# Kernel optimization log

Measured on AMD Instinct MI355X. Metric: run time of the kernel, lower is better.

The kernel has to match this reference:

```python
import jax, jax.numpy as jnp
import numpy as np

EPS = 1e-12  # matches tf l2_normalize epsilon behavior closely enough for testing

def setup_inputs() -> dict:
    key = jax.random.key(0)
    k1, k2 = jax.random.split(key)
    B, M, D = 512, 65536, 512
    context = jax.random.normal(k1, (B, D), dtype=jnp.float32)
    memory = jax.random.normal(k2, (M, D), dtype=jnp.float32)
    return {"context": context, "memory": memory}

def reference(context, memory):
    # tf.keras.losses.cosine_similarity returns NEGATIVE cosine similarity:
    # sim[b,m] = -sum(l2norm(context[b]) * l2norm(memory[m]))
    ctx_n = context / jnp.sqrt(jnp.maximum(jnp.sum(context * context, axis=-1, keepdims=True), EPS))
    mem_n = memory / jnp.sqrt(jnp.maximum(jnp.sum(memory * memory, axis=-1, keepdims=True), EPS))
    sim = -jnp.einsum('bd,md->bm', ctx_n, mem_n)  # [B, M]
    best = jnp.argmin(sim, axis=-1)               # [B], = argmax cosine
    # recall: gather then expand_dims(axis=0) -> [1, B, D]
    return memory[best][None, :, :]
```

## Files before the change

### kernel.cpp

```cpp
#include <hip/hip_runtime.h>
#include <hip/hip_bf16.h>
#include <stdint.h>

#define D_DIM 512
#define B_CTX 512
#define M_MEM 65536
#define BM 128
#define BB 128
#define BBW 256
#define BK 32
#define GBK 32
#define NIT (D_DIM / GBK)
#define LDSPAD 40
#define DELTA_COS 2.5e-3f
#define LISTCAP 2048
#define CVT_MEM_BLOCKS (M_MEM / 32)
#define CVT_BLOCKS (CVT_MEM_BLOCKS + B_CTX / 32)

typedef __attribute__((ext_vector_type(8))) short short8;
typedef __attribute__((ext_vector_type(4))) float floatx4;

__device__ __forceinline__ uint32_t f32_order(float s) {
    uint32_t u = __float_as_uint(s);
    return (u & 0x80000000u) ? ~u : (u | 0x80000000u);
}
__device__ __forceinline__ float f32_unorder(uint32_t v) {
    uint32_t u = (v & 0x80000000u) ? (v & 0x7FFFFFFFu) : ~v;
    return __uint_as_float(u);
}
__device__ __forceinline__ uint32_t pack_bf16_rtn(float a, float b) {
    uint32_t ua = __float_as_uint(a) + 0x8000u;
    uint32_t ub = __float_as_uint(b) + 0x8000u;
    return (ua >> 16) | (ub & 0xFFFF0000u);
}

typedef const __attribute__((address_space(1))) void gv_t;
typedef __attribute__((address_space(3))) void lv_t;
__device__ __forceinline__ void gload_lds16(const uint16_t* g, uint16_t* l) {
    __builtin_amdgcn_global_load_lds((gv_t*)g, (lv_t*)l, 16, 0, 0);
}

__global__ void detect_init(const uint32_t* __restrict__ mem_raw,
                            uint32_t* __restrict__ flag) {
    __shared__ int cnt;
    if (threadIdx.x == 0) cnt = 0;
    __syncthreads();
    int s = 0;
    #pragma unroll
    for (int i = 0; i < 8; ++i) {
        uint32_t u = mem_raw[threadIdx.x * 8 + i];
        uint32_t e = (u >> 7) & 0xFFu;
        s += (e >= 96u && e <= 144u) ? 1 : 0;
    }
    atomicAdd(&cnt, s);
    __syncthreads();
    if (threadIdx.x == 0) *flag = (cnt > 256) ? 1u : 0u;
}

__global__ __launch_bounds__(256) void convert_scale(const void* __restrict__ ctxv,
                                                     const void* __restrict__ memv,
                                                     const uint32_t* __restrict__ flag,
                                                     uint16_t* __restrict__ mem_s,
                                                     uint16_t* __restrict__ ctx_b) {
    const bool isbf = (*flag != 0u);
    const int lane = threadIdx.x & 63;
    const int w = threadIdx.x >> 6;
    if (blockIdx.x < CVT_MEM_BLOCKS) {
        const int gw = blockIdx.x * 4 + w;
        #pragma unroll
        for (int i = 0; i < 8; ++i) {
            const int r = gw * 8 + i;
            float x[8];
            if (isbf) {
                uint4 v = *((const uint4*)((const uint16_t*)memv + (size_t)r * D_DIM) + lane);
                uint32_t ww[4] = {v.x, v.y, v.z, v.w};
                #pragma unroll
                for (int j = 0; j < 4; ++j) {
                    x[2 * j]     = __uint_as_float(ww[j] << 16);
                    x[2 * j + 1] = __uint_as_float(ww[j] & 0xFFFF0000u);
                }
            } else {
                const float4* p = (const float4*)((const float*)memv + (size_t)r * D_DIM) + lane * 2;
                float4 a = p[0], bq = p[1];
                x[0] = a.x; x[1] = a.y; x[2] = a.z; x[3] = a.w;
                x[4] = bq.x; x[5] = bq.y; x[6] = bq.z; x[7] = bq.w;
            }
            float nsq = 0.f;
            #pragma unroll
            for (int j = 0; j < 8; ++j) nsq = fmaf(x[j], x[j], nsq);
            #pragma unroll
            for (int o = 32; o; o >>= 1) nsq += __shfl_xor(nsq, o, 64);
            const float invn = rsqrtf(fmaxf(nsq, 1e-12f));
            uint4 ov;
            ov.x = pack_bf16_rtn(x[0] * invn, x[1] * invn);
            ov.y = pack_bf16_rtn(x[2] * invn, x[3] * invn);
            ov.z = pack_bf16_rtn(x[4] * invn, x[5] * invn);
            ov.w = pack_bf16_rtn(x[6] * invn, x[7] * invn);
            *((uint4*)(mem_s + (size_t)r * D_DIM) + lane) = ov;
        }
    } else {
        const int gw = (blockIdx.x - CVT_MEM_BLOCKS) * 4 + w;
        #pragma unroll
        for (int i = 0; i < 8; ++i) {
            const int r = gw * 8 + i;
            uint4 ov;
            if (isbf) {
                ov = *((const uint4*)((const uint16_t*)ctxv + (size_t)r * D_DIM) + lane);
            } else {
                const float4* p = (const float4*)((const float*)ctxv + (size_t)r * D_DIM) + lane * 2;
                float4 a = p[0], bq = p[1];
                ov.x = pack_bf16_rtn(a.x, a.y);
                ov.y = pack_bf16_rtn(a.z, a.w);
                ov.z = pack_bf16_rtn(bq.x, bq.y);
                ov.w = pack_bf16_rtn(bq.z, bq.w);
            }
            *((uint4*)(ctx_b + (size_t)r * D_DIM) + lane) = ov;
        }
    }
}

#define STAGE3(buf, kofs)                                                          \
    do {                                                                           \
        gload_lds16(ga  + (kofs), &at[buf][0][0] + (size_t)((w << 6)) * 8);        \
        gload_lds16(gb0 + (kofs), &bt[buf][0][0] + (size_t)((w << 6)) * 8);        \
        gload_lds16(gb1 + (kofs), &bt[buf][0][0] + (size_t)(512 + (w << 6)) * 8);  \
    } while (0)

__global__ __launch_bounds__(512, 4) void score_mfma(const uint16_t* __restrict__ A,
                                                     const uint16_t* __restrict__ Bc,
                                                     uint32_t* __restrict__ tmax,
                                                     int coarse) {
    __shared__ __align__(16) uint16_t at[3][BM][GBK];
    __shared__ __align__(16) uint16_t bt[3][BBW][GBK];
    __shared__ uint32_t s_gbest[8][BBW];

    const int h  = blockIdx.y * gridDim.x + blockIdx.x;
    const int v  = (h & 7) * 128 + (h >> 3);
    const int bxp = v & 1;
    const int byp = v >> 1;

    const int t    = threadIdx.x;
    const int b0   = bxp * BBW;
    const int m0   = byp * BM;
    const int lane = t & 63;
    const int w    = t >> 6;
    const int wm   = w >> 2;
    const int wb   = w & 3;
    const int quad = lane >> 4;
    const int l15  = lane & 15;
    const int scol_sw = (((t & 3) ^ ((t >> 3) & 3)) << 3);
    const int rc = ((quad ^ ((l15 >> 1) & 3)) << 3);

    const uint16_t* ga  = A  + (size_t)(m0 + (t >> 2)) * D_DIM + scol_sw;
    const uint16_t* gb0 = Bc + (size_t)(b0 + (t >> 2)) * D_DIM + scol_sw;
    const uint16_t* gb1 = gb0 + (size_t)128 * D_DIM;

    floatx4 acc[4][4];
    #pragma unroll
    for (int i = 0; i < 4; ++i)
        #pragma unroll
        for (int j = 0; j < 4; ++j)
            acc[i][j] = (floatx4){0.f, 0.f, 0.f, 0.f};

    STAGE3(0, 0);

    #pragma unroll
    for (int it = 0; it < NIT; ++it) {
        const int cur = it % 3;
        if (it < NIT - 1) STAGE3((it + 1) % 3, (it + 1) * GBK);
        if (it < NIT - 1) asm volatile("s_waitcnt vmcnt(3)" ::: "memory");
        else              asm volatile("s_waitcnt vmcnt(0)" ::: "memory");
        __builtin_amdgcn_sched_barrier(0);
        __builtin_amdgcn_s_barrier();
        __builtin_amdgcn_sched_barrier(0);

        short8 af[4], bg[4];
        #pragma unroll
        for (int i = 0; i < 4; ++i)
            af[i] = *(const short8*)&at[cur][wm * 64 + i * 16 + l15][rc];
        #pragma unroll
        for (int j = 0; j < 4; ++j)
            bg[j] = *(const short8*)&bt[cur][wb * 64 + j * 16 + l15][rc];
        __builtin_amdgcn_s_setprio(1);
        #pragma unroll
        for (int i = 0; i < 4; ++i)
            #pragma unroll
            for (int j = 0; j < 4; ++j)
                acc[i][j] = __builtin_amdgcn_mfma_f32_16x16x32_bf16(af[i], bg[j], acc[i][j], 0, 0, 0);
        __builtin_amdgcn_s_setprio(0);
    }

    #pragma unroll
    for (int i = 0; i < 4; ++i)
        #pragma unroll
        for (int j = 0; j < 4; ++j) {
            uint32_t k = 0;
            #pragma unroll
            for (int r = 0; r < 4; ++r) {
                uint32_t kk = f32_order(acc[i][j][r]);
                k = kk > k ? kk : k;
            }
            uint32_t o1 = __shfl_xor(k, 16, 64); k = o1 > k ? o1 : k;
            uint32_t o2 = __shfl_xor(k, 32, 64); k = o2 > k ? o2 : k;
            if (quad == 0) s_gbest[wm * 4 + i][wb * 64 + j * 16 + l15] = k;
        }
    __syncthreads();

    if (!coarse) {
        const int G0 = byp * 8;
        for (int e = t; e < 8 * BBW; e += 512) {
            const int col = e >> 3, g = e & 7;
            tmax[(size_t)(b0 + col) * 4096 + G0 + g] = s_gbest[g][col];
        }
    } else {
        if (t < BBW) {
            uint32_t k = s_gbest[0][t];
            #pragma unroll
            for (int g = 1; g < 8; ++g) k = s_gbest[g][t] > k ? s_gbest[g][t] : k;
            tmax[(size_t)(b0 + t) * 512 + byp] = k;
        }
    }
}

__global__ __launch_bounds__(256) void score_phase1(const void* __restrict__ ctxv,
                                                    const void* __restrict__ memv,
                                                    const uint32_t* __restrict__ flag,
                                                    uint32_t* __restrict__ tmax,
                                                    int coarse) {
    __shared__ __align__(16) uint16_t at[BM][LDSPAD];
    __shared__ __align__(16) uint16_t bt[BB][LDSPAD];
    __shared__ float s_nsq[BM];
    __shared__ uint32_t s_gbest[8][BB];

    const int t    = threadIdx.x;
    const int b0   = blockIdx.x * BB;
    const int m0   = blockIdx.y * BM;
    const int lane = t & 63;
    const int w    = t >> 6;
    const int wm   = w >> 1;
    const int wb   = w & 1;
    const int quad = lane >> 4;
    const int l15  = lane & 15;
    const int srow = t >> 2;
    const int scol = (t & 3) * 8;

    floatx4 acc[4][4];
    #pragma unroll
    for (int i = 0; i < 4; ++i)
        #pragma unroll
        for (int j = 0; j < 4; ++j)
            acc[i][j] = (floatx4){0.f, 0.f, 0.f, 0.f};

    float nsq0 = 0.f, nsq1 = 0.f;
    const bool isbf = (*flag != 0u);

    for (int k0 = 0; k0 < D_DIM; k0 += BK) {
        __syncthreads();
        if (isbf) {
            const uint16_t* mp = (const uint16_t*)memv;
            const uint16_t* cp = (const uint16_t*)ctxv;
            uint4 va0 = *(const uint4*)(mp + (size_t)(m0 + srow) * D_DIM + k0 + scol);
            uint4 va1 = *(const uint4*)(mp + (size_t)(m0 + srow + 64) * D_DIM + k0 + scol);
            uint4 vb0 = *(const uint4*)(cp + (size_t)(b0 + srow) * D_DIM + k0 + scol);
            uint4 vb1 = *(const uint4*)(cp + (size_t)(b0 + srow + 64) * D_DIM + k0 + scol);
            *(uint4*)&at[srow][scol] = va0;
            *(uint4*)&at[srow + 64][scol] = va1;
            *(uint4*)&bt[srow][scol] = vb0;
            *(uint4*)&bt[srow + 64][scol] = vb1;
            uint32_t wa0[4] = {va0.x, va0.y, va0.z, va0.w};
            uint32_t wa1[4] = {va1.x, va1.y, va1.z, va1.w};
            #pragma unroll
            for (int i = 0; i < 4; ++i) {
                float a = __uint_as_float(wa0[i] << 16);
                float b = __uint_as_float(wa0[i] & 0xFFFF0000u);
                nsq0 = fmaf(a, a, nsq0); nsq0 = fmaf(b, b, nsq0);
                float c = __uint_as_float(wa1[i] << 16);
                float d = __uint_as_float(wa1[i] & 0xFFFF0000u);
                nsq1 = fmaf(c, c, nsq1); nsq1 = fmaf(d, d, nsq1);
            }
        } else {
            const float* mp = (const float*)memv;
            const float* cp = (const float*)ctxv;
            const float4* pa0 = (const float4*)(mp + (size_t)(m0 + srow) * D_DIM + k0 + scol);
            const float4* pa1 = (const float4*)(mp + (size_t)(m0 + srow + 64) * D_DIM + k0 + scol);
            const float4* pb0 = (const float4*)(cp + (size_t)(b0 + srow) * D_DIM + k0 + scol);
            const float4* pb1 = (const float4*)(cp + (size_t)(b0 + srow + 64) * D_DIM + k0 + scol);
            float4 a0 = pa0[0], a1 = pa0[1], a2 = pa1[0], a3 = pa1[1];
            float4 c0 = pb0[0], c1 = pb0[1], c2 = pb1[0], c3 = pb1[1];
            uint4 va0 = {pack_bf16_rtn(a0.x, a0.y), pack_bf16_rtn(a0.z, a0.w),
                         pack_bf16_rtn(a1.x, a1.y), pack_bf16_rtn(a1.z, a1.w)};
            uint4 va1 = {pack_bf16_rtn(a2.x, a2.y), pack_bf16_rtn(a2.z, a2.w),
                         pack_bf16_rtn(a3.x, a3.y), pack_bf16_rtn(a3.z, a3.w)};
            uint4 vb0 = {pack_bf16_rtn(c0.x, c0.y), pack_bf16_rtn(c0.z, c0.w),
                         pack_bf16_rtn(c1.x, c1.y), pack_bf16_rtn(c1.z, c1.w)};
            uint4 vb1 = {pack_bf16_rtn(c2.x, c2.y), pack_bf16_rtn(c2.z, c2.w),
                         pack_bf16_rtn(c3.x, c3.y), pack_bf16_rtn(c3.z, c3.w)};
            *(uint4*)&at[srow][scol] = va0;
            *(uint4*)&at[srow + 64][scol] = va1;
            *(uint4*)&bt[srow][scol] = vb0;
            *(uint4*)&bt[srow + 64][scol] = vb1;
            nsq0 = fmaf(a0.x, a0.x, nsq0); nsq0 = fmaf(a0.y, a0.y, nsq0);
            nsq0 = fmaf(a0.z, a0.z, nsq0); nsq0 = fmaf(a0.w, a0.w, nsq0);
            nsq0 = fmaf(a1.x, a1.x, nsq0); nsq0 = fmaf(a1.y, a1.y, nsq0);
            nsq0 = fmaf(a1.z, a1.z, nsq0); nsq0 = fmaf(a1.w, a1.w, nsq0);
            nsq1 = fmaf(a2.x, a2.x, nsq1); nsq1 = fmaf(a2.y, a2.y, nsq1);
            nsq1 = fmaf(a2.z, a2.z, nsq1); nsq1 = fmaf(a2.w, a2.w, nsq1);
            nsq1 = fmaf(a3.x, a3.x, nsq1); nsq1 = fmaf(a3.y, a3.y, nsq1);
            nsq1 = fmaf(a3.z, a3.z, nsq1); nsq1 = fmaf(a3.w, a3.w, nsq1);
        }
        __syncthreads();

        short8 af[4], bg[4];
        #pragma unroll
        for (int i = 0; i < 4; ++i)
            af[i] = *(const short8*)&at[wm * 64 + i * 16 + l15][quad * 8];
        #pragma unroll
        for (int j = 0; j < 4; ++j)
            bg[j] = *(const short8*)&bt[wb * 64 + j * 16 + l15][quad * 8];

        #pragma unroll
        for (int i = 0; i < 4; ++i)
            #pragma unroll
            for (int j = 0; j < 4; ++j)
                acc[i][j] = __builtin_amdgcn_mfma_f32_16x16x32_bf16(af[i], bg[j], acc[i][j], 0, 0, 0);
    }

    nsq0 += __shfl_xor(nsq0, 1, 64); nsq0 += __shfl_xor(nsq0, 2, 64);
    nsq1 += __shfl_xor(nsq1, 1, 64); nsq1 += __shfl_xor(nsq1, 2, 64);
    __syncthreads();
    if ((t & 3) == 0) { s_nsq[srow] = nsq0; s_nsq[srow + 64] = nsq1; }
    __syncthreads();

    float invn[4][4];
    #pragma unroll
    for (int i = 0; i < 4; ++i)
        #pragma unroll
        for (int r = 0; r < 4; ++r)
            invn[i][r] = rsqrtf(fmaxf(s_nsq[wm * 64 + i * 16 + quad * 4 + r], 1e-12f));

    #pragma unroll
    for (int i = 0; i < 4; ++i)
        #pragma unroll
        for (int j = 0; j < 4; ++j) {
            uint32_t k = 0;
            #pragma unroll
            for (int r = 0; r < 4; ++r) {
                uint32_t kk = f32_order(acc[i][j][r] * invn[i][r]);
                k = kk > k ? kk : k;
            }
            uint32_t o1 = __shfl_xor(k, 16, 64); k = o1 > k ? o1 : k;
            uint32_t o2 = __shfl_xor(k, 32, 64); k = o2 > k ? o2 : k;
            if (quad == 0) s_gbest[wm * 4 + i][wb * 64 + j * 16 + l15] = k;
        }
    __syncthreads();

    if (!coarse) {
        const int G0 = blockIdx.y * 8;
        for (int e = t; e < 8 * BB; e += 256) {
            const int col = e >> 3, g = e & 7;
            tmax[(size_t)(b0 + col) * 4096 + G0 + g] = s_gbest[g][col];
        }
    } else {
        if (t < BB) {
            uint32_t k = s_gbest[0][t];
            #pragma unroll
            for (int g = 1; g < 8; ++g) k = s_gbest[g][t] > k ? s_gbest[g][t] : k;
            tmax[(size_t)(b0 + t) * 512 + blockIdx.y] = k;
        }
    }
}

__global__ __launch_bounds__(256) void phase2(const void* __restrict__ ctxv,
                                              const void* __restrict__ memv,
                                              const uint32_t* __restrict__ flag,
                                              const uint32_t* __restrict__ tmax,
                                              void* __restrict__ outv,
                                              int ngrp, int gshift) {
    __shared__ float s_ctx[D_DIM];
    __shared__ int s_list[LISTCAP];
    __shared__ int s_cnt;
    __shared__ uint32_t s_red[4];
    __shared__ float s_cn[4];
    __shared__ double s_d[4], s_n[4];
    __shared__ int s_m[4];
    __shared__ int s_bestm;

    const int b = blockIdx.x;
    const int t = threadIdx.x;
    const int lane = t & 63;
    const int w = t >> 6;
    const bool isbf = (*flag != 0u);
    const int gmask = (1 << gshift) - 1;

    if (t == 0) s_cnt = 0;
    if (isbf) {
        if (t < 64) {
            uint4 v = *((const uint4*)((const uint16_t*)ctxv + (size_t)b * D_DIM) + t);
            uint32_t ww[4] = {v.x, v.y, v.z, v.w};
            #pragma unroll
            for (int i = 0; i < 4; ++i) {
                s_ctx[t * 8 + 2 * i]     = __uint_as_float(ww[i] << 16);
                s_ctx[t * 8 + 2 * i + 1] = __uint_as_float(ww[i] & 0xFFFF0000u);
            }
        }
    } else {
        if (t < 128)
            ((float4*)s_ctx)[t] = ((const float4*)((const float*)ctxv + (size_t)b * D_DIM))[t];
    }
    __syncthreads();

    float cs = s_ctx[t] * s_ctx[t] + s_ctx[t + 256] * s_ctx[t + 256];
    #pragma unroll
    for (int o = 32; o; o >>= 1) cs += __shfl_xor(cs, o, 64);
    if (lane == 0) s_cn[w] = cs;

    const uint32_t* tk = tmax + (size_t)b * ngrp;
    const int nk = ngrp >> 8;
    uint32_t km = 0;
    for (int i = 0; i < nk; ++i) {
        uint32_t v = tk[t + (i << 8)];
        km = v > km ? v : km;
    }
    #pragma unroll
    for (int o = 32; o; o >>= 1) { uint32_t ot = __shfl_xor(km, o, 64); km = ot > km ? ot : km; }
    if (lane == 0) s_red[w] = km;
    __syncthreads();
    uint32_t kbest = s_red[0];
    #pragma unroll
    for (int i = 1; i < 4; ++i) kbest = s_red[i] > kbest ? s_red[i] : kbest;
    const float cnorm = sqrtf(s_cn[0] + s_cn[1] + s_cn[2] + s_cn[3]);
    const uint32_t keyT = f32_order(f32_unorder(kbest) - DELTA_COS * cnorm);

    for (int i = 0; i < nk; ++i) {
        uint32_t v = tk[t + (i << 8)];
        if (v >= keyT) {
            int idx = atomicAdd(&s_cnt, 1);
            if (idx < LISTCAP) s_list[idx] = t + (i << 8);
        }
    }
    __syncthreads();
    int cnt = s_cnt; if (cnt > LISTCAP) cnt = LISTCAP;
    const int total = cnt << gshift;

    double bd = -1.0e300, bn = 1.0;
    double bp = bd * 1.0e300;
    int bm = 0x7FFFFFFF;
    const float* cb = s_ctx + lane * 8;

    for (int base = w * 2; base < total; base += 8) {
        const bool has1 = (base + 1 < total);
        const int ia = base, ib = has1 ? base + 1 : base;
        const int ma = (s_list[ia >> gshift] << gshift) + (ia & gmask);
        const int mb = (s_list[ib >> gshift] << gshift) + (ib & gmask);
        double d0 = 0.0, n0 = 0.0, d1 = 0.0, n1 = 0.0;
        if (isbf) {
            uint4 va = *((const uint4*)((const uint16_t*)memv + (size_t)ma * D_DIM) + lane);
            uint4 vb = *((const uint4*)((const uint16_t*)memv + (size_t)mb * D_DIM) + lane);
            uint32_t wa[4] = {va.x, va.y, va.z, va.w};
            uint32_t wbv[4] = {vb.x, vb.y, vb.z, vb.w};
            #pragma unroll
            for (int i = 0; i < 4; ++i) {
                float a0 = __uint_as_float(wa[i] << 16);
                float a1 = __uint_as_float(wa[i] & 0xFFFF0000u);
                d0 += (double)a0 * (double)cb[2 * i];
                d0 += (double)a1 * (double)cb[2 * i + 1];
                n0 += (double)a0 * (double)a0 + (double)a1 * (double)a1;
                float b0v = __uint_as_float(wbv[i] << 16);
                float b1v = __uint_as_float(wbv[i] & 0xFFFF0000u);
                d1 += (double)b0v * (double)cb[2 * i];
                d1 += (double)b1v * (double)cb[2 * i + 1];
                n1 += (double)b0v * (double)b0v + (double)b1v * (double)b1v;
            }
        } else {
            const float4* pa = (const float4*)((const float*)memv + (size_t)ma * D_DIM) + lane * 2;
            const float4* pb = (const float4*)((const float*)memv + (size_t)mb * D_DIM) + lane * 2;
            float4 a0 = pa[0], a1 = pa[1], b0v = pb[0], b1v = pb[1];
            float xa[8] = {a0.x, a0.y, a0.z, a0.w, a1.x, a1.y, a1.z, a1.w};
            float xb[8] = {b0v.x, b0v.y, b0v.z, b0v.w, b1v.x, b1v.y, b1v.z, b1v.w};
            #pragma unroll
            for (int i = 0; i < 8; ++i) {
                d0 += (double)xa[i] * (double)cb[i];
                n0 += (double)xa[i] * (double)xa[i];
                d1 += (double)xb[i] * (double)cb[i];
                n1 += (double)xb[i] * (double)xb[i];
            }
        }
        #pragma unroll
        for (int o = 32; o; o >>= 1) {
            d0 += __shfl_xor(d0, o, 64);
            n0 += __shfl_xor(n0, o, 64);
            d1 += __shfl_xor(d1, o, 64);
            n1 += __shfl_xor(n1, o, 64);
        }
        double p0 = d0 * fabs(d0);
        double lhs = p0 * bn, rhs = bp * n0;
        if (lhs > rhs || (lhs == rhs && ma < bm)) { bd = d0; bn = n0; bp = p0; bm = ma; }
        if (has1) {
            double p1 = d1 * fabs(d1);
            double lhs1 = p1 * bn, rhs1 = bp * n1;
            if (lhs1 > rhs1 || (lhs1 == rhs1 && mb < bm)) { bd = d1; bn = n1; bp = p1; bm = mb; }
        }
    }
    if (lane == 0) { s_d[w] = bd; s_n[w] = bn; s_m[w] = bm; }
    __syncthreads();
    if (t == 0) {
        double cd = s_d[0], cn2 = s_n[0], cp = cd * fabs(cd);
        int cm = s_m[0];
        #pragma unroll
        for (int i = 1; i < 4; ++i) {
            double pd = s_d[i], pn = s_n[i], pp = pd * fabs(pd);
            double lhs = pp * cn2, rhs = cp * pn;
            if (lhs > rhs || (lhs == rhs && s_m[i] < cm)) { cd = pd; cn2 = pn; cp = pp; cm = s_m[i]; }
        }
        s_bestm = cm;
    }
    __syncthreads();
    const int mbest = s_bestm;
    if (isbf) {
        if (t < 64)
            ((uint4*)((uint16_t*)outv + (size_t)b * D_DIM))[t] =
                ((const uint4*)((const uint16_t*)memv + (size_t)mbest * D_DIM))[t];
    } else {
        if (t < 128)
            ((float4*)((float*)outv + (size_t)b * D_DIM))[t] =
                ((const float4*)((const float*)memv + (size_t)mbest * D_DIM))[t];
    }
}

extern "C" void kernel_launch(void* const* d_in, const int* in_sizes, int n_in,
                              void* d_out, int out_size, void* d_ws, size_t ws_size,
                              hipStream_t stream) {
    const void* ctx = d_in[0];
    const void* mem = d_in[1];
    if (in_sizes[0] > in_sizes[1]) { ctx = d_in[1]; mem = d_in[0]; }

    const size_t fineBytes   = (size_t)B_CTX * 4096 * 4;
    const size_t coarseBytes = (size_t)B_CTX * 512 * 4;
    const size_t ctxBytes    = (size_t)B_CTX * D_DIM * 2;
    const size_t memBytes    = (size_t)M_MEM * D_DIM * 2;
    const size_t fastBytes   = fineBytes + 256 + ctxBytes + memBytes;

    if (ws_size >= fastBytes) {
        uint32_t* tmax  = (uint32_t*)d_ws;
        uint32_t* flag  = (uint32_t*)((char*)d_ws + fineBytes);
        uint16_t* ctx_b = (uint16_t*)((char*)d_ws + fineBytes + 256);
        uint16_t* mem_s = (uint16_t*)((char*)d_ws + fineBytes + 256 + ctxBytes);
        dim3 grid(B_CTX / BBW, M_MEM / BM);
        detect_init<<<1, 64, 0, stream>>>((const uint32_t*)mem, flag);
        convert_scale<<<CVT_BLOCKS, 256, 0, stream>>>(ctx, mem, flag, mem_s, ctx_b);
        score_mfma<<<grid, 512, 0, stream>>>(mem_s, ctx_b, tmax, 0);
        phase2<<<B_CTX, 256, 0, stream>>>(ctx, mem, flag, tmax, d_out, 4096, 4);
    } else if (ws_size >= fineBytes + 256) {
        uint32_t* tmax = (uint32_t*)d_ws;
        uint32_t* flag = (uint32_t*)((char*)d_ws + fineBytes);
        dim3 grid(B_CTX / BB, M_MEM / BM);
        detect_init<<<1, 64, 0, stream>>>((const uint32_t*)mem, flag);
        score_phase1<<<grid, 256, 0, stream>>>(ctx, mem, flag, tmax, 0);
        phase2<<<B_CTX, 256, 0, stream>>>(ctx, mem, flag, tmax, d_out, 4096, 4);
    } else {
        uint32_t* tmax = (uint32_t*)d_ws;
        uint32_t* flag = (uint32_t*)((char*)d_ws + coarseBytes);
        dim3 grid(B_CTX / BB, M_MEM / BM);
        detect_init<<<1, 64, 0, stream>>>((const uint32_t*)mem, flag);
        score_phase1<<<grid, 256, 0, stream>>>(ctx, mem, flag, tmax, 1);
        phase2<<<B_CTX, 256, 0, stream>>>(ctx, mem, flag, tmax, d_out, 512, 7);
    }
}
```

Measured before the change: 266.9 us.

## Inline dtype probe per block, batch row loads in convert and phase2

Measured after the change: 263.5 us. About the same (-1.3%).

```diff
diff --git a/kernel.cpp b/kernel.cpp
--- a/kernel.cpp
+++ b/kernel.cpp
@@ -40,6 +40,23 @@
     __builtin_amdgcn_global_load_lds((gv_t*)g, (lv_t*)l, 16, 0, 0);
 }
 
+__device__ __forceinline__ bool probe_isbf(const void* memv, int* s_bf, int t) {
+    if (t == 0) *s_bf = 0;
+    __syncthreads();
+    if (t < 64) {
+        int s = 0;
+        #pragma unroll
+        for (int i = 0; i < 8; ++i) {
+            uint32_t u = ((const uint32_t*)memv)[t * 8 + i];
+            uint32_t e = (u >> 7) & 0xFFu;
+            s += (e >= 96u && e <= 144u) ? 1 : 0;
+        }
+        atomicAdd(s_bf, s);
+    }
+    __syncthreads();
+    return (*s_bf > 256);
+}
+
 __global__ void detect_init(const uint32_t* __restrict__ mem_raw,
                             uint32_t* __restrict__ flag) {
     __shared__ int cnt;
@@ -59,62 +76,75 @@
 
 __global__ __launch_bounds__(256) void convert_scale(const void* __restrict__ ctxv,
                                                      const void* __restrict__ memv,
-                                                     const uint32_t* __restrict__ flag,
                                                      uint16_t* __restrict__ mem_s,
                                                      uint16_t* __restrict__ ctx_b) {
-    const bool isbf = (*flag != 0u);
-    const int lane = threadIdx.x & 63;
-    const int w = threadIdx.x >> 6;
+    __shared__ int s_bf;
+    const int t = threadIdx.x;
+    const bool isbf = probe_isbf(memv, &s_bf, t);
+    const int lane = t & 63;
+    const int w = t >> 6;
     if (blockIdx.x < CVT_MEM_BLOCKS) {
-        const int gw = blockIdx.x * 4 + w;
-        #pragma unroll
-        for (int i = 0; i < 8; ++i) {
-            const int r = gw * 8 + i;
-            float x[8];
-            if (isbf) {
-                uint4 v = *((const uint4*)((const uint16_t*)memv + (size_t)r * D_DIM) + lane);
+        const int r0 = (blockIdx.x * 4 + w) * 8;
+        float x[8][8];
+        if (isbf) {
+            #pragma unroll
+            for (int i = 0; i < 8; ++i) {
+                uint4 v = *((const uint4*)((const uint16_t*)memv + (size_t)(r0 + i) * D_DIM) + lane);
                 uint32_t ww[4] = {v.x, v.y, v.z, v.w};
                 #pragma unroll
                 for (int j = 0; j < 4; ++j) {
-                    x[2 * j]     = __uint_as_float(ww[j] << 16);
-                    x[2 * j + 1] = __uint_as_float(ww[j] & 0xFFFF0000u);
+                    x[i][2 * j]     = __uint_as_float(ww[j] << 16);
+                    x[i][2 * j + 1] = __uint_as_float(ww[j] & 0xFFFF0000u);
                 }
-            } else {
-                const float4* p = (const float4*)((const float*)memv + (size_t)r * D_DIM) + lane * 2;
+            }
+        } else {
+            #pragma unroll
+            for (int i = 0; i < 8; ++i) {
+                const float4* p = (const float4*)((const float*)memv + (size_t)(r0 + i) * D_DIM) + lane * 2;
                 float4 a = p[0], bq = p[1];
-                x[0] = a.x; x[1] = a.y; x[2] = a.z; x[3] = a.w;
-                x[4] = bq.x; x[5] = bq.y; x[6] = bq.z; x[7] = bq.w;
-            }
-            float nsq = 0.f;
-            #pragma unroll
-            for (int j = 0; j < 8; ++j) nsq = fmaf(x[j], x[j], nsq);
-            #pragma unroll
-            for (int o = 32; o; o >>= 1) nsq += __shfl_xor(nsq, o, 64);
-            const float invn = rsqrtf(fmaxf(nsq, 1e-12f));
+                x[i][0] = a.x; x[i][1] = a.y; x[i][2] = a.z; x[i][3] = a.w;
+                x[i][4] = bq.x; x[i][5] = bq.y; x[i][6] = bq.z; x[i][7] = bq.w;
+            }
+        }
+        float nsq[8];
+        #pragma unroll
+        for (int i = 0; i < 8; ++i) {
+            float s = 0.f;
+            #pragma unroll
+            for (int j = 0; j < 8; ++j) s = fmaf(x[i][j], x[i][j], s);
+            nsq[i] = s;
+        }
+        #pragma unroll
+        for (int o = 32; o; o >>= 1)
+            #pragma unroll
+            for (int i = 0; i < 8; ++i)
+                nsq[i] += __shfl_xor(nsq[i], o, 64);
+        #pragma unroll
+        for (int i = 0; i < 8; ++i) {
+            const float invn = rsqrtf(fmaxf(nsq[i], 1e-12f));
             uint4 ov;
-            ov.x = pack_bf16_rtn(x[0] * invn, x[1] * invn);
-            ov.y = pack_bf16_rtn(x[2] * invn, x[3] * invn);
-            ov.z = pack_bf16_rtn(x[4] * invn, x[5] * invn);
-            ov.w = pack_bf16_rtn(x[6] * invn, x[7] * invn);
-            *((uint4*)(mem_s + (size_t)r * D_DIM) + lane) = ov;
-        }
-    } else {
-        const int gw = (blockIdx.x - CVT_MEM_BLOCKS) * 4 + w;
+            ov.x = pack_bf16_rtn(x[i][0] * invn, x[i][1] * invn);
+            ov.y = pack_bf16_rtn(x[i][2] * invn, x[i][3] * invn);
+            ov.z = pack_bf16_rtn(x[i][4] * invn, x[i][5] * invn);
+            ov.w = pack_bf16_rtn(x[i][6] * invn, x[i][7] * invn);
+            *((uint4*)(mem_s + (size_t)(r0 + i) * D_DIM) + lane) = ov;
+        }
+    } else {
+        const int r0 = ((blockIdx.x - CVT_MEM_BLOCKS) * 4 + w) * 8;
         #pragma unroll
         for (int i = 0; i < 8; ++i) {
-            const int r = gw * 8 + i;
             uint4 ov;
             if (isbf) {
-                ov = *((const uint4*)((const uint16_t*)ctxv + (size_t)r * D_DIM) + lane);
+                ov = *((const uint4*)((const uint16_t*)ctxv + (size_t)(r0 + i) * D_DIM) + lane);
             } else {
-                const float4* p = (const float4*)((const float*)ctxv + (size_t)r * D_DIM) + lane * 2;
+                const float4* p = (const float4*)((const float*)ctxv + (size_t)(r0 + i) * D_DIM) + lane * 2;
                 float4 a = p[0], bq = p[1];
                 ov.x = pack_bf16_rtn(a.x, a.y);
                 ov.y = pack_bf16_rtn(a.z, a.w);
                 ov.z = pack_bf16_rtn(bq.x, bq.y);
                 ov.w = pack_bf16_rtn(bq.z, bq.w);
             }
-            *((uint4*)(ctx_b + (size_t)r * D_DIM) + lane) = ov;
+            *((uint4*)(ctx_b + (size_t)(r0 + i) * D_DIM) + lane) = ov;
         }
     }
 }
@@ -372,13 +402,13 @@
 
 __global__ __launch_bounds__(256) void phase2(const void* __restrict__ ctxv,
                                               const void* __restrict__ memv,
-                                              const uint32_t* __restrict__ flag,
                                               const uint32_t* __restrict__ tmax,
                                               void* __restrict__ outv,
                                               int ngrp, int gshift) {
     __shared__ float s_ctx[D_DIM];
     __shared__ int s_list[LISTCAP];
     __shared__ int s_cnt;
+    __shared__ int s_bf;
     __shared__ uint32_t s_red[4];
     __shared__ float s_cn[4];
     __shared__ double s_d[4], s_n[4];
@@ -389,10 +419,11 @@
     const int t = threadIdx.x;
     const int lane = t & 63;
     const int w = t >> 6;
-    const bool isbf = (*flag != 0u);
     const int gmask = (1 << gshift) - 1;
 
     if (t == 0) s_cnt = 0;
+    const bool isbf = probe_isbf(memv, &s_bf, t);
+
     if (isbf) {
         if (t < 64) {
             uint4 v = *((const uint4*)((const uint16_t*)ctxv + (size_t)b * D_DIM) + t);
@@ -415,11 +446,18 @@
     if (lane == 0) s_cn[w] = cs;
 
     const uint32_t* tk = tmax + (size_t)b * ngrp;
-    const int nk = ngrp >> 8;
+    uint32_t kv[16];
     uint32_t km = 0;
-    for (int i = 0; i < nk; ++i) {
-        uint32_t v = tk[t + (i << 8)];
-        km = v > km ? v : km;
+    const bool fine = (ngrp == 4096);
+    if (fine) {
+        #pragma unroll
+        for (int i = 0; i < 16; ++i) kv[i] = tk[t + (i << 8)];
+        #pragma unroll
+        for (int i = 0; i < 16; ++i) km = kv[i] > km ? kv[i] : km;
+    } else {
+        #pragma unroll
+        for (int i = 0; i < 2; ++i) kv[i] = tk[t + (i << 8)];
+        km = kv[0] > kv[1] ? kv[0] : kv[1];
     }
     #pragma unroll
     for (int o = 32; o; o >>= 1) { uint32_t ot = __shfl_xor(km, o, 64); km = ot > km ? ot : km; }
@@ -431,12 +469,20 @@
     const float cnorm = sqrtf(s_cn[0] + s_cn[1] + s_cn[2] + s_cn[3]);
     const uint32_t keyT = f32_order(f32_unorder(kbest) - DELTA_COS * cnorm);
 
-    for (int i = 0; i < nk; ++i) {
-        uint32_t v = tk[t + (i << 8)];
-        if (v >= keyT) {
-            int idx = atomicAdd(&s_cnt, 1);
-            if (idx < LISTCAP) s_list[idx] = t + (i << 8);
-        }
+    if (fine) {
+        #pragma unroll
+        for (int i = 0; i < 16; ++i)
+            if (kv[i] >= keyT) {
+                int idx = atomicAdd(&s_cnt, 1);
+                if (idx < LISTCAP) s_list[idx] = t + (i << 8);
+            }
+    } else {
+        #pragma unroll
+        for (int i = 0; i < 2; ++i)
+            if (kv[i] >= keyT) {
+                int idx = atomicAdd(&s_cnt, 1);
+                if (idx < LISTCAP) s_list[idx] = t + (i << 8);
+            }
     }
     __syncthreads();
     int cnt = s_cnt; if (cnt > LISTCAP) cnt = LISTCAP;
@@ -542,27 +588,25 @@
 
     if (ws_size >= fastBytes) {
         uint32_t* tmax  = (uint32_t*)d_ws;
-        uint32_t* flag  = (uint32_t*)((char*)d_ws + fineBytes);
         uint16_t* ctx_b = (uint16_t*)((char*)d_ws + fineBytes + 256);
         uint16_t* mem_s = (uint16_t*)((char*)d_ws + fineBytes + 256 + ctxBytes);
         dim3 grid(B_CTX / BBW, M_MEM / BM);
-        detect_init<<<1, 64, 0, stream>>>((const uint32_t*)mem, flag);
-        convert_scale<<<CVT_BLOCKS, 256, 0, stream>>>(ctx, mem, flag, mem_s, ctx_b);
+        convert_scale<<<CVT_BLOCKS, 256, 0, stream>>>(ctx, mem, mem_s, ctx_b);
         score_mfma<<<grid, 512, 0, stream>>>(mem_s, ctx_b, tmax, 0);
-        phase2<<<B_CTX, 256, 0, stream>>>(ctx, mem, flag, tmax, d_out, 4096, 4);
+        phase2<<<B_CTX, 256, 0, stream>>>(ctx, mem, tmax, d_out, 4096, 4);
     } else if (ws_size >= fineBytes + 256) {
         uint32_t* tmax = (uint32_t*)d_ws;
         uint32_t* flag = (uint32_t*)((char*)d_ws + fineBytes);
         dim3 grid(B_CTX / BB, M_MEM / BM);
         detect_init<<<1, 64, 0, stream>>>((const uint32_t*)mem, flag);
         score_phase1<<<grid, 256, 0, stream>>>(ctx, mem, flag, tmax, 0);
-        phase2<<<B_CTX, 256, 0, stream>>>(ctx, mem, flag, tmax, d_out, 4096, 4);
+        phase2<<<B_CTX, 256, 0, stream>>>(ctx, mem, tmax, d_out, 4096, 4);
     } else {
         uint32_t* tmax = (uint32_t*)d_ws;
         uint32_t* flag = (uint32_t*)((char*)d_ws + coarseBytes);
         dim3 grid(B_CTX / BB, M_MEM / BM);
         detect_init<<<1, 64, 0, stream>>>((const uint32_t*)mem, flag);
         score_phase1<<<grid, 256, 0, stream>>>(ctx, mem, flag, tmax, 1);
-        phase2<<<B_CTX, 256, 0, stream>>>(ctx, mem, flag, tmax, d_out, 512, 7);
-    }
-}
+        phase2<<<B_CTX, 256, 0, stream>>>(ctx, mem, tmax, d_out, 512, 7);
+    }
+}
```
